# Kernel optimization log

Hardware: AMD Instinct MI355X
Metric: run time of the kernel (lower is better)

Reference implementation:

```python
import jax, jax.numpy as jnp
import numpy as np

# Scale constants (production tokenizer-style)
P = 1_048_576   # total flat byte-params (sum of token lengths over vocab)
E = 8_388_608   # occurrence edges: (token-instance, byte-within-token) pairs
T = 4_194_304   # text length in bytes
N = 2_097_152   # number of token instances (valid_tokens)
INIT_STD = 0.02


def setup_inputs() -> dict:
    key = jax.random.key(0)
    k1, k2, k3, k4 = jax.random.split(key, 4)
    flat_params = jax.random.normal(k1, (P,), dtype=jnp.float32) * INIT_STD
    # occ_param_idx[e] = offset[token_id_e] + byte_idx_e  (index into flat param vector)
    occ_param_idx = jax.random.randint(k2, (E,), 0, P, dtype=jnp.int32)
    # occ_byte_pos[e] = start_pos_e + byte_idx_e  (absolute byte position in text)
    occ_byte_pos = jax.random.randint(k3, (E,), 0, T, dtype=jnp.int32)
    # occ_token_idx[e] = which token instance this byte occurrence belongs to
    occ_token_idx = jax.random.randint(k4, (E,), 0, N, dtype=jnp.int32)
    return {
        "flat_params": flat_params,
        "occ_param_idx": occ_param_idx,
        "occ_byte_pos": occ_byte_pos,
        "occ_token_idx": occ_token_idx,
        "text_len": T,
        "num_tokens": N,
    }


def reference(flat_params, occ_param_idx, occ_byte_pos, occ_token_idx, text_len, num_tokens):
    # 1) gather per-occurrence byte params
    vals = flat_params[occ_param_idx]                                      # [E]
    # 2) scatter-add into byte positions: sum and count per byte
    byte_sum = jax.ops.segment_sum(vals, occ_byte_pos, num_segments=text_len)            # [T]
    byte_cnt = jax.ops.segment_sum(jnp.ones_like(vals), occ_byte_pos, num_segments=text_len)  # [T]
    # 3) mean per byte (0 where no token covers the byte, as in the torch code)
    byte_w = jnp.where(byte_cnt > 0, byte_sum / jnp.maximum(byte_cnt, 1.0), 0.0)          # [T]
    # 4) each token's position = sum of byte weights over its span
    positions = jax.ops.segment_sum(byte_w[occ_byte_pos], occ_token_idx, num_segments=num_tokens)  # [N]
    return positions
```

## Files before the change

kernel.cpp:

```cpp
#include <hip/hip_runtime.h>


typedef unsigned long long u64;
typedef unsigned int uint;

constexpr int NB   = 512;
constexpr int PPB  = 8192;
constexpr int NB2  = 512;
constexpr int TOKB = 4096;
constexpr int CAP  = 17408;
constexpr int CAP2 = 17408;

constexpr float V_SCALE = 2097152.0f;
constexpr float V_INV   = 1.0f / 2097152.0f;
constexpr float W_SCALE = 1048576.0f;
constexpr float W_INV   = 1.0f / 1048576.0f;

__device__ __forceinline__ void wave_scan512(const uint* hist, uint* lbase,
                                             int t) {
    if (t < 64) {
        uint h[8];
        uint run = 0;
        #pragma unroll
        for (int j = 0; j < 8; ++j) { h[j] = run; run += hist[t * 8 + j]; }
        uint tot = run, inc = tot;
        #pragma unroll
        for (int d = 1; d < 64; d <<= 1) {
            uint up = __shfl_up(inc, d, 64);
            if (t >= d) inc += up;
        }
        uint excl = inc - tot;
        #pragma unroll
        for (int j = 0; j < 8; ++j) lbase[t * 8 + j] = excl + h[j];
        if (t == 63) lbase[512] = inc;
    }
}

constexpr int A_THREADS = 1024;
constexpr int A_EPT     = 8;
constexpr int A_CHUNK   = A_THREADS * A_EPT;

__global__ __launch_bounds__(A_THREADS) void phaseA(
    const float* __restrict__ fp, const int* __restrict__ pidx,
    const int* __restrict__ bpos, const int* __restrict__ tidx,
    u64* __restrict__ recs, uint* __restrict__ gcur, int E)
{
    __shared__ u64 stage[A_CHUNK];
    __shared__ uint hist[NB], lcur[NB], gbase[NB], lbase[NB + 1];
    int t = threadIdx.x;
    if (t < NB) { hist[t] = 0u; lcur[t] = 0u; }
    __syncthreads();

    int base_e = blockIdx.x * A_CHUNK + t * A_EPT;
    bool vec = (base_e + A_EPT) <= E;

    int4 b0, b1, k0, k1;
    float v0=0,v1=0,v2=0,v3=0,v4=0,v5=0,v6=0,v7=0;
    if (vec) {
        int4 p0 = *(const int4*)(pidx + base_e);
        int4 p1 = *(const int4*)(pidx + base_e + 4);
        b0 = *(const int4*)(bpos + base_e);
        b1 = *(const int4*)(bpos + base_e + 4);
        k0 = *(const int4*)(tidx + base_e);
        k1 = *(const int4*)(tidx + base_e + 4);
        v0 = fp[p0.x]; v1 = fp[p0.y]; v2 = fp[p0.z]; v3 = fp[p0.w];
        v4 = fp[p1.x]; v5 = fp[p1.y]; v6 = fp[p1.z]; v7 = fp[p1.w];
        atomicAdd(&hist[((uint)b0.x) >> 13], 1u);
        atomicAdd(&hist[((uint)b0.y) >> 13], 1u);
        atomicAdd(&hist[((uint)b0.z) >> 13], 1u);
        atomicAdd(&hist[((uint)b0.w) >> 13], 1u);
        atomicAdd(&hist[((uint)b1.x) >> 13], 1u);
        atomicAdd(&hist[((uint)b1.y) >> 13], 1u);
        atomicAdd(&hist[((uint)b1.z) >> 13], 1u);
        atomicAdd(&hist[((uint)b1.w) >> 13], 1u);
    } else {
        for (int j = 0; j < A_EPT; ++j) {
            int e = base_e + j;
            if (e < E) atomicAdd(&hist[((uint)bpos[e]) >> 13], 1u);
        }
    }
    __syncthreads();

    wave_scan512(hist, lbase, t);
    if (t >= 512) gbase[t - 512] = atomicAdd(&gcur[t - 512], hist[t - 512]);
    __syncthreads();

    auto emit = [&](int p, int tk, float v) {
        uint b = ((uint)p) >> 13;
        int fx = (int)rintf(v * V_SCALE);
        u64 rec = (u64)(uint)(p & (PPB - 1))
                | ((u64)(uint)tk << 13)
                | ((u64)(uint)(fx + (1 << 20)) << 34)
                | ((u64)b << 55);
        uint off = lbase[b] + atomicAdd(&lcur[b], 1u);
        stage[off] = rec;
    };
    if (vec) {
        emit(b0.x, k0.x, v0); emit(b0.y, k0.y, v1);
        emit(b0.z, k0.z, v2); emit(b0.w, k0.w, v3);
        emit(b1.x, k1.x, v4); emit(b1.y, k1.y, v5);
        emit(b1.z, k1.z, v6); emit(b1.w, k1.w, v7);
    } else {
        for (int j = 0; j < A_EPT; ++j) {
            int e = base_e + j;
            if (e < E) emit(bpos[e], tidx[e], fp[pidx[e]]);
        }
    }
    __syncthreads();

    uint total = lbase[NB];
    for (uint i = t; i < total; i += A_THREADS) {
        u64 rc = stage[i];
        int b = (int)(rc >> 55);
        uint dst = gbase[b] + (i - lbase[b]);
        if (dst < (uint)CAP)
            recs[(size_t)b * CAP + dst] = rc;
    }
}

constexpr int C_THREADS = 1024;
constexpr int C_CHUNK   = 8192;
constexpr int C_MAXCH   = (CAP + C_CHUNK - 1) / C_CHUNK;

__global__ __launch_bounds__(C_THREADS) void phaseC(
    const u64* __restrict__ recs, const uint* __restrict__ gcur,
    uint* __restrict__ rec2, uint* __restrict__ gcur2)
{
    __shared__ uint acc[PPB];
    __shared__ uint stage2[C_CHUNK];
    __shared__ uint histc[C_MAXCH][NB2];
    __shared__ uint lcur[NB2], gb[NB2], lbase[NB2 + 1];
    int t = threadIdx.x;
    int b = blockIdx.x;
    for (int i = t; i < PPB; i += C_THREADS) acc[i] = 0u;
    for (int i = t; i < C_MAXCH * NB2; i += C_THREADS) (&histc[0][0])[i] = 0u;
    if (t < NB2) lcur[t] = 0u;
    __syncthreads();

    uint n = min(gcur[b], (uint)CAP);
    const u64* r = recs + (size_t)b * CAP;

    auto process = [&](u64 rc, uint ch) {
        uint pos = (uint)rc & (PPB - 1);
        int fx = (int)((uint)(rc >> 34) & 0x1FFFFFu) - (1 << 20);
        atomicAdd(&acc[pos], (uint)((1 << 26) + fx));
        atomicAdd(&histc[ch][(uint)(rc >> 25) & 0x1FFu], 1u);
    };
    uint np = n >> 1;
    for (uint i = t; i < np; i += C_THREADS) {
        ulonglong2 rr = ((const ulonglong2*)r)[i];
        uint ch = (2u * i) / C_CHUNK;
        process(rr.x, ch); process(rr.y, ch);
    }
    for (uint i = 2u * np + t; i < n; i += C_THREADS) process(r[i], i / C_CHUNK);
    __syncthreads();

    if (t >= 512) {
        int tb = t - 512;
        uint tot = histc[0][tb];
        #pragma unroll
        for (int c = 1; c < C_MAXCH; ++c) tot += histc[c][tb];
        gb[tb] = atomicAdd(&gcur2[tb], tot);
    }

    uint ch = 0;
    for (uint c0 = 0; c0 < n; c0 += C_CHUNK, ++ch) {
        uint m = min((uint)C_CHUNK, n - c0);
        wave_scan512(histc[ch], lbase, t);
        __syncthreads();
        for (uint i = t; i < m; i += C_THREADS) {
            u64 rc = r[c0 + i];
            uint pos = (uint)rc & (PPB - 1);
            uint tok = (uint)(rc >> 13) & 0x1FFFFFu;
            uint a = acc[pos];
            uint c = (a + (1u << 25)) >> 26;
            int s = (int)(a - (c << 26));
            float w = (float)s * V_INV / (float)c;
            int wfx = (int)rintf(w * W_SCALE);
            uint tb = tok >> 12;
            uint off = lbase[tb] + atomicAdd(&lcur[tb], 1u);
            stage2[off] = (tok & (TOKB - 1)) | ((uint)wfx << 12);
        }
        __syncthreads();
        int w = t >> 6, lane = t & 63;
        for (int tb = w; tb < NB2; tb += 16) {
            uint base = lbase[tb];
            uint len  = lbase[tb + 1] - base;
            uint g    = gb[tb];
            for (uint j = lane; j < len; j += 64) {
                uint dst = g + j;
                if (dst < (uint)CAP2)
                    rec2[(size_t)tb * CAP2 + dst] = stage2[base + j];
            }
        }
        __syncthreads();
        if (t < NB2) { gb[t] += histc[ch][t]; lcur[t] = 0u; }
        __syncthreads();
    }
}

constexpr int D_THREADS = 1024;

__global__ __launch_bounds__(D_THREADS) void phaseD(
    const uint* __restrict__ rec2, const uint* __restrict__ gcur2,
    float* __restrict__ out, int N)
{
    __shared__ int facc[TOKB];
    int t = threadIdx.x;
    int b = blockIdx.x;
    for (int i = t; i < TOKB; i += D_THREADS) facc[i] = 0;
    __syncthreads();
    uint n = min(gcur2[b], (uint)CAP2);
    const uint* r = rec2 + (size_t)b * CAP2;
    uint nq = n >> 2;
    for (uint i = t; i < nq; i += D_THREADS) {
        uint4 q = ((const uint4*)r)[i];
        atomicAdd(&facc[q.x & (TOKB - 1)], ((int)q.x) >> 12);
        atomicAdd(&facc[q.y & (TOKB - 1)], ((int)q.y) >> 12);
        atomicAdd(&facc[q.z & (TOKB - 1)], ((int)q.z) >> 12);
        atomicAdd(&facc[q.w & (TOKB - 1)], ((int)q.w) >> 12);
    }
    for (uint i = 4u * nq + t; i < n; i += D_THREADS) {
        uint rc = r[i];
        atomicAdd(&facc[rc & (TOKB - 1)], ((int)rc) >> 12);
    }
    __syncthreads();
    int base = b * TOKB;
    for (int i = t; i < TOKB; i += D_THREADS) {
        int idx = base + i;
        if (idx < N) out[idx] = (float)facc[i] * W_INV;
    }
}

__global__ void fb_scatter(const float* __restrict__ fp,
                           const int* __restrict__ pidx,
                           const int* __restrict__ bpos,
                           u64* __restrict__ bacc, int E) {
    int e = blockIdx.x * blockDim.x + threadIdx.x;
    if (e < E) {
        float v = fp[pidx[e]];
        long long fx = (long long)rintf(v * 4294967296.0f);
        atomicAdd(&bacc[bpos[e]], (1ULL << 39) + (u64)fx);
    }
}

__global__ void fb_tokens(const u64* __restrict__ bacc,
                          const int* __restrict__ bpos,
                          const int* __restrict__ tidx,
                          float* __restrict__ out, int E) {
    int e = blockIdx.x * blockDim.x + threadIdx.x;
    if (e < E) {
        u64 v = bacc[bpos[e]];
        long long cnt = (long long)((v + (1ULL << 38)) >> 39);
        long long s   = (long long)(v - ((u64)cnt << 39));
        atomicAdd(&out[tidx[e]], (float)s * (1.0f / 4294967296.0f) / (float)cnt);
    }
}

extern "C" void kernel_launch(void* const* d_in, const int* in_sizes, int n_in,
                              void* d_out, int out_size, void* d_ws, size_t ws_size,
                              hipStream_t stream) {
    const float* flat_params   = (const float*)d_in[0];
    const int*   occ_param_idx = (const int*)d_in[1];
    const int*   occ_byte_pos  = (const int*)d_in[2];
    const int*   occ_token_idx = (const int*)d_in[3];

    const int E = in_sizes[1];
    const int N = out_size;

    const size_t REC_BYTES  = (size_t)NB  * CAP  * 8;
    const size_t REC2_BYTES = (size_t)NB2 * CAP2 * 4;
    const size_t NEED = 4096 + REC_BYTES + REC2_BYTES;

    if (ws_size >= NEED && N <= NB2 * TOKB) {
        uint* gcur  = (uint*)d_ws;
        uint* gcur2 = (uint*)((char*)d_ws + 2048);
        u64* recs = (u64*)((char*)d_ws + 4096);
        uint* rec2 = (uint*)((char*)d_ws + 4096 + REC_BYTES);

        hipMemsetAsync(d_ws, 0, 4096, stream);

        int gridA = (E + A_CHUNK - 1) / A_CHUNK;
        phaseA<<<gridA, A_THREADS, 0, stream>>>(flat_params, occ_param_idx,
                                                occ_byte_pos, occ_token_idx,
                                                recs, gcur, E);
        phaseC<<<NB, C_THREADS, 0, stream>>>(recs, gcur, rec2, gcur2);
        phaseD<<<NB2, D_THREADS, 0, stream>>>(rec2, gcur2, (float*)d_out, N);
    } else {
        u64* bacc = (u64*)d_ws;
        hipMemsetAsync(bacc, 0, (size_t)4194304 * 8, stream);
        hipMemsetAsync(d_out, 0, (size_t)N * sizeof(float), stream);
        int gridE = (E + 255) / 256;
        fb_scatter<<<gridE, 256, 0, stream>>>(flat_params, occ_param_idx,
                                              occ_byte_pos, bacc, E);
        fb_tokens<<<gridE, 256, 0, stream>>>(bacc, occ_byte_pos,
                                             occ_token_idx, (float*)d_out, E);
    }
}
```

Baseline: 265.1 us.

## Halve token bins to 256 and use nontemporal loads/stores for streaming buffers

```diff
diff --git a/kernel.cpp b/kernel.cpp
--- a/kernel.cpp
+++ b/kernel.cpp
@@ -3,18 +3,21 @@
 
 typedef unsigned long long u64;
 typedef unsigned int uint;
+typedef int  vi4  __attribute__((ext_vector_type(4)));
+typedef u64  vu64x2 __attribute__((ext_vector_type(2)));
+typedef uint vu4  __attribute__((ext_vector_type(4)));
 
 constexpr int NB   = 512;
 constexpr int PPB  = 8192;
-constexpr int NB2  = 512;
-constexpr int TOKB = 4096;
+constexpr int NB2  = 256;
+constexpr int TOKB = 8192;
 constexpr int CAP  = 17408;
-constexpr int CAP2 = 17408;
+constexpr int CAP2 = 34816;
 
 constexpr float V_SCALE = 2097152.0f;
 constexpr float V_INV   = 1.0f / 2097152.0f;
-constexpr float W_SCALE = 1048576.0f;
-constexpr float W_INV   = 1.0f / 1048576.0f;
+constexpr float W_SCALE = 524288.0f;
+constexpr float W_INV   = 1.0f / 524288.0f;
 
 __device__ __forceinline__ void wave_scan512(const uint* hist, uint* lbase,
                                              int t) {
@@ -33,6 +36,26 @@
         #pragma unroll
         for (int j = 0; j < 8; ++j) lbase[t * 8 + j] = excl + h[j];
         if (t == 63) lbase[512] = inc;
+    }
+}
+
+__device__ __forceinline__ void wave_scan256(const uint* hist, uint* lbase,
+                                             int t) {
+    if (t < 64) {
+        uint h[4];
+        uint run = 0;
+        #pragma unroll
+        for (int j = 0; j < 4; ++j) { h[j] = run; run += hist[t * 4 + j]; }
+        uint tot = run, inc = tot;
+        #pragma unroll
+        for (int d = 1; d < 64; d <<= 1) {
+            uint up = __shfl_up(inc, d, 64);
+            if (t >= d) inc += up;
+        }
+        uint excl = inc - tot;
+        #pragma unroll
+        for (int j = 0; j < 4; ++j) lbase[t * 4 + j] = excl + h[j];
+        if (t == 63) lbase[256] = inc;
     }
 }
 
@@ -54,15 +77,15 @@
     int base_e = blockIdx.x * A_CHUNK + t * A_EPT;
     bool vec = (base_e + A_EPT) <= E;
 
-    int4 b0, b1, k0, k1;
+    vi4 b0, b1, k0, k1;
     float v0=0,v1=0,v2=0,v3=0,v4=0,v5=0,v6=0,v7=0;
     if (vec) {
-        int4 p0 = *(const int4*)(pidx + base_e);
-        int4 p1 = *(const int4*)(pidx + base_e + 4);
-        b0 = *(const int4*)(bpos + base_e);
-        b1 = *(const int4*)(bpos + base_e + 4);
-        k0 = *(const int4*)(tidx + base_e);
-        k1 = *(const int4*)(tidx + base_e + 4);
+        vi4 p0 = __builtin_nontemporal_load((const vi4*)(pidx + base_e));
+        vi4 p1 = __builtin_nontemporal_load((const vi4*)(pidx + base_e + 4));
+        b0 = __builtin_nontemporal_load((const vi4*)(bpos + base_e));
+        b1 = __builtin_nontemporal_load((const vi4*)(bpos + base_e + 4));
+        k0 = __builtin_nontemporal_load((const vi4*)(tidx + base_e));
+        k1 = __builtin_nontemporal_load((const vi4*)(tidx + base_e + 4));
         v0 = fp[p0.x]; v1 = fp[p0.y]; v2 = fp[p0.z]; v3 = fp[p0.w];
         v4 = fp[p1.x]; v5 = fp[p1.y]; v6 = fp[p1.z]; v7 = fp[p1.w];
         atomicAdd(&hist[((uint)b0.x) >> 13], 1u);
@@ -114,7 +137,7 @@
         int b = (int)(rc >> 55);
         uint dst = gbase[b] + (i - lbase[b]);
         if (dst < (uint)CAP)
-            recs[(size_t)b * CAP + dst] = rc;
+            __builtin_nontemporal_store(rc, &recs[(size_t)b * CAP + dst]);
     }
 }
 
@@ -144,18 +167,18 @@
         uint pos = (uint)rc & (PPB - 1);
         int fx = (int)((uint)(rc >> 34) & 0x1FFFFFu) - (1 << 20);
         atomicAdd(&acc[pos], (uint)((1 << 26) + fx));
-        atomicAdd(&histc[ch][(uint)(rc >> 25) & 0x1FFu], 1u);
+        atomicAdd(&histc[ch][(uint)(rc >> 26) & 0xFFu], 1u);
     };
     uint np = n >> 1;
     for (uint i = t; i < np; i += C_THREADS) {
-        ulonglong2 rr = ((const ulonglong2*)r)[i];
+        vu64x2 rr = __builtin_nontemporal_load(((const vu64x2*)r) + i);
         uint ch = (2u * i) / C_CHUNK;
         process(rr.x, ch); process(rr.y, ch);
     }
     for (uint i = 2u * np + t; i < n; i += C_THREADS) process(r[i], i / C_CHUNK);
     __syncthreads();
 
-    if (t >= 512) {
+    if (t >= 512 && t < 512 + NB2) {
         int tb = t - 512;
         uint tot = histc[0][tb];
         #pragma unroll
@@ -166,10 +189,10 @@
     uint ch = 0;
     for (uint c0 = 0; c0 < n; c0 += C_CHUNK, ++ch) {
         uint m = min((uint)C_CHUNK, n - c0);
-        wave_scan512(histc[ch], lbase, t);
+        wave_scan256(histc[ch], lbase, t);
         __syncthreads();
         for (uint i = t; i < m; i += C_THREADS) {
-            u64 rc = r[c0 + i];
+            u64 rc = __builtin_nontemporal_load(r + c0 + i);
             uint pos = (uint)rc & (PPB - 1);
             uint tok = (uint)(rc >> 13) & 0x1FFFFFu;
             uint a = acc[pos];
@@ -177,9 +200,9 @@
             int s = (int)(a - (c << 26));
             float w = (float)s * V_INV / (float)c;
             int wfx = (int)rintf(w * W_SCALE);
-            uint tb = tok >> 12;
+            uint tb = tok >> 13;
             uint off = lbase[tb] + atomicAdd(&lcur[tb], 1u);
-            stage2[off] = (tok & (TOKB - 1)) | ((uint)wfx << 12);
+            stage2[off] = (tok & (TOKB - 1)) | ((uint)wfx << 13);
         }
         __syncthreads();
         int w = t >> 6, lane = t & 63;
@@ -190,7 +213,8 @@
             for (uint j = lane; j < len; j += 64) {
                 uint dst = g + j;
                 if (dst < (uint)CAP2)
-                    rec2[(size_t)tb * CAP2 + dst] = stage2[base + j];
+                    __builtin_nontemporal_store(stage2[base + j],
+                                                &rec2[(size_t)tb * CAP2 + dst]);
             }
         }
         __syncthreads();
@@ -214,21 +238,22 @@
     const uint* r = rec2 + (size_t)b * CAP2;
     uint nq = n >> 2;
     for (uint i = t; i < nq; i += D_THREADS) {
-        uint4 q = ((const uint4*)r)[i];
-        atomicAdd(&facc[q.x & (TOKB - 1)], ((int)q.x) >> 12);
-        atomicAdd(&facc[q.y & (TOKB - 1)], ((int)q.y) >> 12);
-        atomicAdd(&facc[q.z & (TOKB - 1)], ((int)q.z) >> 12);
-        atomicAdd(&facc[q.w & (TOKB - 1)], ((int)q.w) >> 12);
+        vu4 q = __builtin_nontemporal_load(((const vu4*)r) + i);
+        atomicAdd(&facc[q.x & (TOKB - 1)], ((int)q.x) >> 13);
+        atomicAdd(&facc[q.y & (TOKB - 1)], ((int)q.y) >> 13);
+        atomicAdd(&facc[q.z & (TOKB - 1)], ((int)q.z) >> 13);
+        atomicAdd(&facc[q.w & (TOKB - 1)], ((int)q.w) >> 13);
     }
     for (uint i = 4u * nq + t; i < n; i += D_THREADS) {
         uint rc = r[i];
-        atomicAdd(&facc[rc & (TOKB - 1)], ((int)rc) >> 12);
+        atomicAdd(&facc[rc & (TOKB - 1)], ((int)rc) >> 13);
     }
     __syncthreads();
     int base = b * TOKB;
     for (int i = t; i < TOKB; i += D_THREADS) {
         int idx = base + i;
-        if (idx < N) out[idx] = (float)facc[i] * W_INV;
+        if (idx < N)
+            __builtin_nontemporal_store((float)facc[i] * W_INV, &out[idx]);
     }
 }
 
@@ -278,7 +303,7 @@
         u64* recs = (u64*)((char*)d_ws + 4096);
         uint* rec2 = (uint*)((char*)d_ws + 4096 + REC_BYTES);
 
-        hipMemsetAsync(d_ws, 0, 4096, stream);
+        (void)hipMemsetAsync(d_ws, 0, 4096, stream);
 
         int gridA = (E + A_CHUNK - 1) / A_CHUNK;
         phaseA<<<gridA, A_THREADS, 0, stream>>>(flat_params, occ_param_idx,
@@ -288,8 +313,8 @@
         phaseD<<<NB2, D_THREADS, 0, stream>>>(rec2, gcur2, (float*)d_out, N);
     } else {
         u64* bacc = (u64*)d_ws;
-        hipMemsetAsync(bacc, 0, (size_t)4194304 * 8, stream);
-        hipMemsetAsync(d_out, 0, (size_t)N * sizeof(float), stream);
+        (void)hipMemsetAsync(bacc, 0, (size_t)4194304 * 8, stream);
+        (void)hipMemsetAsync(d_out, 0, (size_t)N * sizeof(float), stream);
         int gridE = (E + 255) / 256;
         fb_scatter<<<gridE, 256, 0, stream>>>(flat_params, occ_param_idx,
                                               occ_byte_pos, bacc, E);
```

Measured after the change: 262.6 us. Within noise of the previous version (-0.9%).
